# Optimization experiments

Hardware: AMD Instinct MI355X
Metric: run time of the kernel (lower is better)

The kernel has to match this reference:

```python
import jax, jax.numpy as jnp
import numpy as np

N, E = 100000, 1600000
IN, H, Z, C = 64, 128, 64, 2


def _glorot(key, fan_in, fan_out):
    s = jnp.sqrt(2.0 / (fan_in + fan_out)).astype(jnp.float32)
    return jax.random.normal(key, (fan_in, fan_out), dtype=jnp.float32) * s


def setup_inputs() -> dict:
    key = jax.random.key(0)
    ks = jax.random.split(key, 16)
    dims = [(IN, H), (H, H), (H, Z), (H, H), (H, Z), (Z, H), (H, H), (H, IN * C)]
    names = ['in', 'mu0', 'mu', 'si0', 'si', 'z', 'd0', 'out']
    inp = {
        'x': jax.random.normal(ks[0], (N, IN), dtype=jnp.float32),
        'eps': jax.random.normal(ks[1], (N, Z), dtype=jnp.float32),
        'edge_index': jax.random.randint(ks[2], (2, E), 0, N, dtype=jnp.int64),
    }
    for i, (nm, (fi, fo)) in enumerate(zip(names, dims)):
        inp[f'w_{nm}'] = _glorot(ks[3 + i], fi, fo)
        inp[f'b_{nm}'] = jnp.zeros((fo,), dtype=jnp.float32)
    return inp


def _gcn(x, W, b, src, dst, dinv):
    # PyG GCNConv: symmetric normalization with self-loops.
    h = x @ W                                      # [N, d_out]
    norm = (dinv[src] * dinv[dst])[:, None]        # [E, 1]
    agg = jax.ops.segment_sum(h[src] * norm, dst, num_segments=N)
    agg = agg + h * (dinv * dinv)[:, None]         # self-loop term (norm = 1/deg)
    return agg + b


def reference(x, edge_index, eps,
              w_in, b_in, w_mu0, b_mu0, w_mu, b_mu,
              w_si0, b_si0, w_si, b_si,
              w_z, b_z, w_d0, b_d0, w_out, b_out):
    src, dst = edge_index[0], edge_index[1]
    deg = jax.ops.segment_sum(jnp.ones((E,), jnp.float32), dst, num_segments=N) + 1.0
    dinv = jax.lax.rsqrt(deg)
    # encode
    h = jax.nn.relu(_gcn(x, w_in, b_in, src, dst, dinv))
    mu = jax.nn.relu(_gcn(h, w_mu0, b_mu0, src, dst, dinv))
    mu = jax.nn.relu(_gcn(mu, w_mu, b_mu, src, dst, dinv))
    si = jax.nn.relu(_gcn(h, w_si0, b_si0, src, dst, dinv))
    si = jax.nn.sigmoid(_gcn(si, w_si, b_si, src, dst, dinv))
    # reparameterize
    z = mu + si * eps
    # decode (first decoder layer has no activation, per the original forward)
    r = _gcn(z, w_z, b_z, src, dst, dinv)
    r = jax.nn.relu(_gcn(r, w_d0, b_d0, src, dst, dinv))
    logits = _gcn(r, w_out, b_out, src, dst, dinv)   # [N, IN*C]
    logits = logits.reshape(-1, C)                   # [N*IN, C]
    return logits, mu, si
```

## Files before the change

kernel.cpp:

```cpp
#include <hip/hip_runtime.h>


typedef short bf16x8 __attribute__((ext_vector_type(8)));
typedef float f32x4 __attribute__((ext_vector_type(4)));

__device__ __forceinline__ ushort f2bf(float f) {
    uint x = __float_as_uint(f);
    uint r = x + 0x7FFFu + ((x >> 16) & 1u);
    return (ushort)(r >> 16);
}
__device__ __forceinline__ float bf2f(ushort h) {
    return __uint_as_float(((uint)h) << 16);
}
__device__ __forceinline__ float dot2bf(uint a, uint b, float c) {
    float d;
    asm("v_dot2_f32_bf16 %0, %1, %2, %3" : "=v"(d) : "v"(a), "v"(b), "v"(c));
    return d;
}

__global__ __launch_bounds__(1024) void counts_kernel(const int* __restrict__ dst,
        int* __restrict__ deg, int* __restrict__ bc0, int E, int NB, int shift) {
    __shared__ int h[8192];
    for (int j = threadIdx.x; j < NB; j += 1024) h[j] = 0;
    __syncthreads();
    int stride = gridDim.x * 1024;
    for (int i = blockIdx.x * 1024 + threadIdx.x; i < E; i += stride) {
        int d = dst[i];
        atomicAdd(&deg[d], 1);
        atomicAdd(&h[d >> shift], 1);
    }
    __syncthreads();
    for (int j = threadIdx.x; j < NB; j += 1024) {
        int v = h[j];
        if (v) atomicAdd(&bc0[j], v);
    }
}

__global__ void dinv_kernel(const int* __restrict__ deg, float* __restrict__ dinv, int N) {
    int i = blockIdx.x * blockDim.x + threadIdx.x;
    if (i < N) dinv[i] = rsqrtf((float)(deg[i] + 1));
}

__global__ __launch_bounds__(1024) void scan_block_kernel(const int* __restrict__ in,
                                                          int* __restrict__ out,
                                                          int* __restrict__ bsum, int n) {
    __shared__ int s[1024];
    int i = blockIdx.x * 1024 + threadIdx.x;
    int v = (i < n) ? in[i] : 0;
    s[threadIdx.x] = v;
    __syncthreads();
    for (int off = 1; off < 1024; off <<= 1) {
        int t = (threadIdx.x >= off) ? s[threadIdx.x - off] : 0;
        __syncthreads();
        s[threadIdx.x] += t;
        __syncthreads();
    }
    if (i < n) out[i] = s[threadIdx.x] - v;
    if (threadIdx.x == 1023) bsum[blockIdx.x] = s[1023];
}

__global__ __launch_bounds__(1024) void scan_partials_kernel(int* __restrict__ bsum, int nb) {
    __shared__ int s[1024];
    int v = (threadIdx.x < nb) ? bsum[threadIdx.x] : 0;
    s[threadIdx.x] = v;
    __syncthreads();
    for (int off = 1; off < 1024; off <<= 1) {
        int t = (threadIdx.x >= off) ? s[threadIdx.x - off] : 0;
        __syncthreads();
        s[threadIdx.x] += t;
        __syncthreads();
    }
    if (threadIdx.x < nb) bsum[threadIdx.x] = s[threadIdx.x] - v;
}

__global__ __launch_bounds__(1024) void scan_add_kernel(int* __restrict__ arr,
                                                        const int* __restrict__ bsum, int n, int total) {
    int i = blockIdx.x * 1024 + threadIdx.x;
    if (i < n) arr[i] += bsum[blockIdx.x];
    if (i == 0) arr[n] = total;
}

__global__ void scatter_kernel(const int* __restrict__ src, const int* __restrict__ dst,
                               const int* __restrict__ bin_start, int* __restrict__ bc1,
                               int2* __restrict__ ebuf, int E, int shift) {
    int i = blockIdx.x * blockDim.x + threadIdx.x;
    if (i < E) {
        int d = dst[i];
        int b = d >> shift;
        int pos = bin_start[b] + atomicAdd(&bc1[b], 1);
        ebuf[pos] = make_int2(src[i], d);
    }
}

__global__ void place2_kernel(const int2* __restrict__ ebuf, const int* __restrict__ row_start,
                              int* __restrict__ cnt, int2* __restrict__ csr,
                              const float* __restrict__ dinv, int E) {
    int i = blockIdx.x * blockDim.x + threadIdx.x;
    if (i < E) {
        int2 e = ebuf[i];
        int pos = row_start[e.y] + atomicAdd(&cnt[e.y], 1);
        csr[pos] = make_int2(e.x, (int)(uint)f2bf(dinv[e.x] * dinv[e.y]));
    }
}

__global__ void rowsum_kernel(const int2* __restrict__ csr, const int* __restrict__ row_start,
                              const float* __restrict__ dinv, float* __restrict__ cvec, int N) {
    int j = blockIdx.x * blockDim.x + threadIdx.x;
    if (j >= N) return;
    float s = dinv[j] * dinv[j];
    int b = row_start[j], e = row_start[j + 1];
    for (int k = b; k < e; ++k) s += bf2f((ushort)((uint)csr[k].y & 0xFFFFu));
    cvec[j] = s;
}

__global__ void wcpack_kernel(const float* __restrict__ w_z, const float* __restrict__ b_z,
                              const float* __restrict__ w_d0,
                              ushort* __restrict__ P_wc, float* __restrict__ bzw) {
    int o = blockIdx.x * 256 + threadIdx.x;
    if (o >= 65 * 128) return;
    int i = o >> 7, j = o & 127;
    float s = 0.f;
    for (int k = 0; k < 128; ++k) {
        float a = (i < 64) ? w_z[i * 128 + k] : b_z[k];
        s = fmaf(a, w_d0[k * 128 + j], s);
    }
    if (i < 64) {
        int c = j >> 4, kb = i >> 5, l = ((i >> 3) & 3) * 16 + (j & 15), e = i & 7;
        P_wc[(size_t)((c * 2 + kb) * 64 + l) * 8 + e] = f2bf(s);
    } else bzw[j] = s;
}

__device__ __forceinline__ void pack_one(const float* __restrict__ W, ushort* __restrict__ P,
                                         int KI, int KO, int idx) {
    if (idx >= KI * KO) return;
    int e = idx & 7, l = (idx >> 3) & 63, t = idx >> 9;
    int KB = KI / 32;
    int c = t / KB, kb = t % KB;
    int k = kb * 32 + ((l >> 4) << 3) + e, col = c * 16 + (l & 15);
    P[idx] = f2bf(W[(size_t)k * KO + col]);
}

__global__ void megapack_kernel(const float* w_in, const float* w_mu0, const float* w_si0,
                                const float* w_mu, const float* w_si, const float* w_out,
                                ushort* P_in, ushort* P_mu0, ushort* P_si0,
                                ushort* P_mu, ushort* P_si, ushort* P_out) {
    int b = blockIdx.x, tid = threadIdx.x;
    if (b < 32)       pack_one(w_in,  P_in,  64, 128,  (b - 0)   * 256 + tid);
    else if (b < 96)  pack_one(w_mu0, P_mu0, 128, 128, (b - 32)  * 256 + tid);
    else if (b < 160) pack_one(w_si0, P_si0, 128, 128, (b - 96)  * 256 + tid);
    else if (b < 192) pack_one(w_mu,  P_mu,  128, 64,  (b - 160) * 256 + tid);
    else if (b < 224) pack_one(w_si,  P_si,  128, 64,  (b - 192) * 256 + tid);
    else              pack_one(w_out, P_out, 128, 128, (b - 224) * 256 + tid);
}

__global__ void cvt8_kernel(const float* __restrict__ in, ushort* __restrict__ out, int n8) {
    int i = blockIdx.x * 256 + threadIdx.x;
    if (i >= n8) return;
    float4 a = ((const float4*)in)[i * 2];
    float4 b = ((const float4*)in)[i * 2 + 1];
    bf16x8 o;
    o[0] = (short)f2bf(a.x); o[1] = (short)f2bf(a.y);
    o[2] = (short)f2bf(a.z); o[3] = (short)f2bf(a.w);
    o[4] = (short)f2bf(b.x); o[5] = (short)f2bf(b.y);
    o[6] = (short)f2bf(b.z); o[7] = (short)f2bf(b.w);
    ((bf16x8*)out)[i] = o;
}

template <int W, int DEPTH>
__device__ __forceinline__ void gather_pairs(float* acc, const ushort* __restrict__ xb,
        const int2* __restrict__ csr, int node, int beg, int end, int sub, int f8) {
    constexpr int SLOTS = 64 / (W / 8);
    for (int base = beg; base < end; base += 2 * SLOTS * DEPTH) {
        int sidx[DEPTH][2];
        uint wv[DEPTH][2];
        #pragma unroll
        for (int d = 0; d < DEPTH; ++d) {
            int e0 = base + 2 * (sub + SLOTS * d), e1 = e0 + 1;
            int2 p0 = csr[e0 < end ? e0 : beg];
            int2 p1 = csr[e1 < end ? e1 : beg];
            sidx[d][0] = (e0 < end) ? p0.x : node;
            sidx[d][1] = (e1 < end) ? p1.x : node;
            wv[d][0] = (e0 < end) ? (uint)p0.y : 0u;
            wv[d][1] = (e1 < end) ? (uint)p1.y : 0u;
        }
        uint4 rv[DEPTH][2];
        #pragma unroll
        for (int d = 0; d < DEPTH; ++d) {
            rv[d][0] = *(const uint4*)(xb + (size_t)sidx[d][0] * W + f8 * 8);
            rv[d][1] = *(const uint4*)(xb + (size_t)sidx[d][1] * W + f8 * 8);
        }
        #pragma unroll
        for (int d = 0; d < DEPTH; ++d) {
            uint wpk = __builtin_amdgcn_perm(wv[d][1], wv[d][0], 0x05040100u);
            uint4 v0 = rv[d][0], v1 = rv[d][1];
            uint t;
            t = __builtin_amdgcn_perm(v1.x, v0.x, 0x05040100u); acc[0] = dot2bf(t, wpk, acc[0]);
            t = __builtin_amdgcn_perm(v1.x, v0.x, 0x07060302u); acc[1] = dot2bf(t, wpk, acc[1]);
            t = __builtin_amdgcn_perm(v1.y, v0.y, 0x05040100u); acc[2] = dot2bf(t, wpk, acc[2]);
            t = __builtin_amdgcn_perm(v1.y, v0.y, 0x07060302u); acc[3] = dot2bf(t, wpk, acc[3]);
            t = __builtin_amdgcn_perm(v1.z, v0.z, 0x05040100u); acc[4] = dot2bf(t, wpk, acc[4]);
            t = __builtin_amdgcn_perm(v1.z, v0.z, 0x07060302u); acc[5] = dot2bf(t, wpk, acc[5]);
            t = __builtin_amdgcn_perm(v1.w, v0.w, 0x05040100u); acc[6] = dot2bf(t, wpk, acc[6]);
            t = __builtin_amdgcn_perm(v1.w, v0.w, 0x07060302u); acc[7] = dot2bf(t, wpk, acc[7]);
        }
    }
}

template <int W, int DEPTH>
__global__ __launch_bounds__(256) void bprop_kernel(const ushort* __restrict__ xb,
        ushort* __restrict__ out, const int* __restrict__ row_start,
        const int2* __restrict__ csr, const float* __restrict__ dinv, int N) {
    constexpr int L = W / 8;
    int wave = threadIdx.x >> 6, lane = threadIdx.x & 63;
    int node = blockIdx.x * 4 + wave;
    if (node >= N) return;
    int sub = lane / L, f8 = lane % L;
    int beg = row_start[node], end = row_start[node + 1];
    float d2 = dinv[node]; d2 *= d2;
    float acc[8] = {};
    gather_pairs<W, DEPTH>(acc, xb, csr, node, beg, end, sub, f8);
    #pragma unroll
    for (int m = L; m < 64; m <<= 1) {
        #pragma unroll
        for (int q = 0; q < 8; ++q) acc[q] += __shfl_xor(acc[q], m);
    }
    if (sub != 0) return;
    bf16x8 sv = *(const bf16x8*)(xb + (size_t)node * W + f8 * 8);
    bf16x8 oz;
    #pragma unroll
    for (int q = 0; q < 8; ++q) oz[q] = (short)f2bf(fmaf(d2, bf2f((ushort)sv[q]), acc[q]));
    *(bf16x8*)(out + (size_t)node * W + f8 * 8) = oz;
}

__global__ __launch_bounds__(256) void mssz_kernel(const ushort* __restrict__ T,
        const int* __restrict__ row_start, const int2* __restrict__ csr,
        const float* __restrict__ dinv, const float* __restrict__ b_mu,
        const float* __restrict__ b_si, const float* __restrict__ eps,
        float* __restrict__ M, float* __restrict__ S, ushort* __restrict__ zb, int N) {
    constexpr int L = 16;
    int wave = threadIdx.x >> 6, lane = threadIdx.x & 63;
    int node = blockIdx.x * 4 + wave;
    if (node >= N) return;
    int sub = lane / L, f8 = lane % L;
    int beg = row_start[node], end = row_start[node + 1];
    float d2 = dinv[node]; d2 *= d2;
    float acc[8] = {};
    gather_pairs<128, 2>(acc, T, csr, node, beg, end, sub, f8);
    #pragma unroll
    for (int m = 16; m < 64; m <<= 1) {
        #pragma unroll
        for (int q = 0; q < 8; ++q) acc[q] += __shfl_xor(acc[q], m);
    }
    if (sub != 0) return;
    bf16x8 sv = *(const bf16x8*)(T + (size_t)node * 128 + f8 * 8);
    #pragma unroll
    for (int q = 0; q < 8; ++q) acc[q] = fmaf(d2, bf2f((ushort)sv[q]), acc[q]);

    bool is_mu = (f8 < 8);
    const float* bp = is_mu ? b_mu : b_si;
    int o = (f8 & 7) * 8;
    float val[8];
    #pragma unroll
    for (int q = 0; q < 8; ++q) {
        float t = acc[q] + bp[o + q];
        val[q] = is_mu ? fmaxf(t, 0.f) : 1.f / (1.f + __expf(-t));
    }
    if (is_mu) {
        *(float4*)&M[(size_t)node * 64 + o]     = make_float4(val[0], val[1], val[2], val[3]);
        *(float4*)&M[(size_t)node * 64 + o + 4] = make_float4(val[4], val[5], val[6], val[7]);
    } else {
        *(float4*)&S[(size_t)node * 64 + o]     = make_float4(val[0], val[1], val[2], val[3]);
        *(float4*)&S[(size_t)node * 64 + o + 4] = make_float4(val[4], val[5], val[6], val[7]);
    }
    float oth[8];
    #pragma unroll
    for (int q = 0; q < 8; ++q) oth[q] = __shfl_xor(val[q], 8);
    if (is_mu) {
        float4 e0v = *(const float4*)&eps[(size_t)node * 64 + o];
        float4 e1v = *(const float4*)&eps[(size_t)node * 64 + o + 4];
        float ev[8] = {e0v.x, e0v.y, e0v.z, e0v.w, e1v.x, e1v.y, e1v.z, e1v.w};
        bf16x8 z;
        #pragma unroll
        for (int q = 0; q < 8; ++q) z[q] = (short)f2bf(fmaf(oth[q], ev[q], val[q]));
        *(bf16x8*)(zb + (size_t)node * 64 + o) = z;
    }
}

__global__ __launch_bounds__(256) void encgemm_kernel(const ushort* __restrict__ PH,
        const bf16x8* __restrict__ Pmu0, const float* __restrict__ b_mu0,
        const bf16x8* __restrict__ Pmu,
        const bf16x8* __restrict__ Psi0, const float* __restrict__ b_si0,
        const bf16x8* __restrict__ Psi,
        ushort* __restrict__ T, int N) {
    constexpr int STR = 136;
    __shared__ __align__(16) ushort Ls[64 * STR];
    int w = threadIdx.x >> 6, l = threadIdx.x & 63;
    int lr = l & 15, lk = l >> 4;
    int rowbase = blockIdx.x * 64;
    int arow = rowbase + w * 16 + lr; if (arow > N - 1) arow = N - 1;

    bf16x8 aph[4];
    const ushort* pp = PH + (size_t)arow * 128 + lk * 8;
    #pragma unroll
    for (int kb = 0; kb < 4; ++kb) aph[kb] = *(const bf16x8*)(pp + kb * 32);

    int crow0 = w * 16 + lk * 4;
    int afrow = w * 16 + lr;

    #pragma unroll
    for (int c = 0; c < 8; ++c) {
        f32x4 acc = {0.f, 0.f, 0.f, 0.f};
        #pragma unroll
        for (int kb = 0; kb < 4; ++kb)
            acc = __builtin_amdgcn_mfma_f32_16x16x32_bf16(aph[kb], Pmu0[((size_t)c * 4 + kb) * 64 + l], acc, 0, 0, 0);
        float bv = b_mu0[c * 16 + lr];
        #pragma unroll
        for (int r = 0; r < 4; ++r)
            Ls[(crow0 + r) * STR + c * 16 + lr] = f2bf(fmaxf(acc[r] + bv, 0.f));
    }
    __syncthreads();
    bf16x8 am[4];
    #pragma unroll
    for (int kb = 0; kb < 4; ++kb) am[kb] = *(const bf16x8*)&Ls[afrow * STR + kb * 32 + lk * 8];
    f32x4 tmu[4];
    #pragma unroll
    for (int c = 0; c < 4; ++c) {
        f32x4 acc = {0.f, 0.f, 0.f, 0.f};
        #pragma unroll
        for (int kb = 0; kb < 4; ++kb)
            acc = __builtin_amdgcn_mfma_f32_16x16x32_bf16(am[kb], Pmu[((size_t)c * 4 + kb) * 64 + l], acc, 0, 0, 0);
        tmu[c] = acc;
    }
    __syncthreads();
    #pragma unroll
    for (int c = 0; c < 8; ++c) {
        f32x4 acc = {0.f, 0.f, 0.f, 0.f};
        #pragma unroll
        for (int kb = 0; kb < 4; ++kb)
            acc = __builtin_amdgcn_mfma_f32_16x16x32_bf16(aph[kb], Psi0[((size_t)c * 4 + kb) * 64 + l], acc, 0, 0, 0);
        float bv = b_si0[c * 16 + lr];
        #pragma unroll
        for (int r = 0; r < 4; ++r)
            Ls[(crow0 + r) * STR + c * 16 + lr] = f2bf(fmaxf(acc[r] + bv, 0.f));
    }
    __syncthreads();
    #pragma unroll
    for (int kb = 0; kb < 4; ++kb) am[kb] = *(const bf16x8*)&Ls[afrow * STR + kb * 32 + lk * 8];
    f32x4 tsi[4];
    #pragma unroll
    for (int c = 0; c < 4; ++c) {
        f32x4 acc = {0.f, 0.f, 0.f, 0.f};
        #pragma unroll
        for (int kb = 0; kb < 4; ++kb)
            acc = __builtin_amdgcn_mfma_f32_16x16x32_bf16(am[kb], Psi[((size_t)c * 4 + kb) * 64 + l], acc, 0, 0, 0);
        tsi[c] = acc;
    }
    __syncthreads();
    #pragma unroll
    for (int c = 0; c < 4; ++c) {
        #pragma unroll
        for (int r = 0; r < 4; ++r) {
            Ls[(crow0 + r) * STR + c * 16 + lr]      = f2bf(tmu[c][r]);
            Ls[(crow0 + r) * STR + 64 + c * 16 + lr] = f2bf(tsi[c][r]);
        }
    }
    __syncthreads();
    for (int idx = threadIdx.x; idx < 64 * 16; idx += 256) {
        int row = idx >> 4, c8 = idx & 15;
        if (rowbase + row < N) {
            bf16x8 vv = *(const bf16x8*)&Ls[row * STR + c8 * 8];
            *(bf16x8*)(T + (size_t)(rowbase + row) * 128 + c8 * 8) = vv;
        }
    }
}

template <int KI, int KO, int EPI, int OUT>
__global__ __launch_bounds__(256) void mgemm_kernel(const ushort* __restrict__ Xb,
                                                    const bf16x8* __restrict__ Wp,
                                                    const float* __restrict__ bias,
                                                    const float* __restrict__ bias2,
                                                    const float* __restrict__ cvec,
                                                    void* __restrict__ outp, int ostride, int N) {
    constexpr int KB = KI / 32;
    constexpr int CT = KO / 16;
    constexpr size_t LSB = (OUT == 1) ? (size_t)64 * KO * 4 : (size_t)64 * KO * 2;
    __shared__ __align__(16) char LsRaw[LSB];

    int w = threadIdx.x >> 6, l = threadIdx.x & 63;
    int lr = l & 15, lk = l >> 4;
    int rowbase = blockIdx.x * 64;
    int r0 = rowbase + w * 16;

    int arow = r0 + lr; if (arow > N - 1) arow = N - 1;
    bf16x8 a[KB];
    const ushort* xp = Xb + (size_t)arow * KI + lk * 8;
    #pragma unroll
    for (int kb = 0; kb < KB; ++kb) a[kb] = *(const bf16x8*)(xp + kb * 32);

    float cv[4];
    if constexpr (EPI == 3) {
        #pragma unroll
        for (int r = 0; r < 4; ++r) {
            int rr = r0 + lk * 4 + r;
            cv[r] = cvec[rr < N ? rr : 0];
        }
    }

    #pragma unroll
    for (int c = 0; c < CT; ++c) {
        f32x4 acc = {0.f, 0.f, 0.f, 0.f};
        #pragma unroll
        for (int kb = 0; kb < KB; ++kb)
            acc = __builtin_amdgcn_mfma_f32_16x16x32_bf16(a[kb], Wp[((size_t)c * KB + kb) * 64 + l], acc, 0, 0, 0);
        int col = c * 16 + lr;
        float bv = 0.f, b2v = 0.f;
        if constexpr (EPI >= 1) bv = bias[col];
        if constexpr (EPI == 3) b2v = bias2[col];
        #pragma unroll
        for (int r = 0; r < 4; ++r) {
            float v = acc[r];
            if constexpr (EPI == 1) v += bv;
            if constexpr (EPI == 2) v = fmaxf(v + bv, 0.f);
            if constexpr (EPI == 3) v = fmaxf(v + cv[r] * bv + b2v, 0.f);
            int rl = w * 16 + lk * 4 + r;
            if constexpr (OUT == 0) ((ushort*)LsRaw)[(size_t)rl * KO + col] = f2bf(v);
            else                    ((float*)LsRaw)[(size_t)rl * KO + col] = v;
        }
    }
    __syncthreads();

    if constexpr (OUT == 0) {
        ushort* o = (ushort*)outp;
        constexpr int CH = 64 * KO / 8;
        for (int idx = threadIdx.x; idx < CH; idx += 256) {
            int row = idx / (KO / 8), c8 = idx % (KO / 8);
            if (rowbase + row < N)
                *(bf16x8*)(o + (size_t)(rowbase + row) * ostride + c8 * 8) = ((const bf16x8*)LsRaw)[idx];
        }
    } else {
        float* o = (float*)outp;
        constexpr int CH = 64 * KO / 4;
        for (int idx = threadIdx.x; idx < CH; idx += 256) {
            int row = idx / (KO / 4), c4 = idx % (KO / 4);
            if (rowbase + row < N)
                *(float4*)(o + (size_t)(rowbase + row) * ostride + c4 * 4) = ((const float4*)LsRaw)[idx];
        }
    }
}

extern "C" void kernel_launch(void* const* d_in, const int* in_sizes, int n_in,
                              void* d_out, int out_size, void* d_ws, size_t ws_size,
                              hipStream_t stream) {
    const float* x    = (const float*)d_in[0];
    const float* eps  = (const float*)d_in[1];
    const int*   ei   = (const int*)d_in[2];
    const float* w_in  = (const float*)d_in[3];  const float* b_in  = (const float*)d_in[4];
    const float* w_mu0 = (const float*)d_in[5];  const float* b_mu0 = (const float*)d_in[6];
    const float* w_mu  = (const float*)d_in[7];  const float* b_mu  = (const float*)d_in[8];
    const float* w_si0 = (const float*)d_in[9];  const float* b_si0 = (const float*)d_in[10];
    const float* w_si  = (const float*)d_in[11]; const float* b_si  = (const float*)d_in[12];
    const float* w_z   = (const float*)d_in[13]; const float* b_z   = (const float*)d_in[14];
    const float* w_d0  = (const float*)d_in[15]; const float* b_d0  = (const float*)d_in[16];
    const float* w_out = (const float*)d_in[17]; const float* b_out = (const float*)d_in[18];

    const int N = in_sizes[0] / 64;
    const int E = in_sizes[2] / 2;
    const int* srcI = ei;
    const int* dstI = ei + E;

    int shift = 4;
    while (((N >> shift) + 1) > 8192) shift++;
    const int NB = (N >> shift) + 1;

    auto align = [](size_t v) { return (v + 255) & ~(size_t)255; };
    char* wsp = (char*)d_ws;
    size_t off = 0;
    int*    deg       = (int*)(wsp + off);    size_t deg_off = off; off = align(off + (size_t)N * 4);
    int*    bc0       = (int*)(wsp + off);    off = align(off + (size_t)NB * 4);
    int*    bc1       = (int*)(wsp + off);    off = align(off + (size_t)NB * 4);
    size_t  zero_span = off - deg_off;
    float*  cvec      = (float*)(wsp + off);  off = align(off + (size_t)N * 4);
    int*    row_start = (int*)(wsp + off);    off = align(off + (size_t)(N + 1) * 4);
    int*    bin_start = (int*)(wsp + off);    off = align(off + (size_t)(NB + 1) * 4);
    int*    bsum      = (int*)(wsp + off);    off = align(off + 1024 * 4);
    float*  dinv      = (float*)(wsp + off);  off = align(off + (size_t)N * 4);
    float*  bzw       = (float*)(wsp + off);  off = align(off + 128 * 4);
    ushort* P_in      = (ushort*)(wsp + off); off = align(off + 64 * 128 * 2);
    ushort* P_mu0     = (ushort*)(wsp + off); off = align(off + 128 * 128 * 2);
    ushort* P_si0     = (ushort*)(wsp + off); off = align(off + 128 * 128 * 2);
    ushort* P_mu      = (ushort*)(wsp + off); off = align(off + 128 * 64 * 2);
    ushort* P_si      = (ushort*)(wsp + off); off = align(off + 128 * 64 * 2);
    ushort* P_wc      = (ushort*)(wsp + off); off = align(off + 64 * 128 * 2);
    ushort* P_out     = (ushort*)(wsp + off); off = align(off + 128 * 128 * 2);
    int2*   csr       = (int2*)(wsp + off);   off = align(off + (size_t)E * 8);
    int2*   ebuf      = (int2*)(wsp + off);   off = align(off + (size_t)E * 8);
    ushort* xb        = (ushort*)ebuf;
    ushort* B1        = (ushort*)(wsp + off); off = align(off + (size_t)N * 128 * 2);
    ushort* B1lo = B1;
    ushort* B1hi = B1 + (size_t)N * 64;

    float* Cc = (float*)d_out;
    float* M  = Cc + (size_t)N * 128;
    float* S  = M + (size_t)N * 64;
    ushort* CcLo = (ushort*)Cc;
    ushort* CcHi = (ushort*)(Cc + (size_t)N * 64);
    ushort* Db   = (ushort*)M;

    const int TB = 256;
    hipMemsetAsync(deg, 0, zero_span, stream);
    counts_kernel<<<256, 1024, 0, stream>>>(dstI, deg, bc0, E, NB, shift);
    dinv_kernel<<<(N + TB - 1) / TB, TB, 0, stream>>>(deg, dinv, N);
    int nbN = (N + 1023) / 1024;
    scan_block_kernel<<<nbN, 1024, 0, stream>>>(deg, row_start, bsum, N);
    scan_partials_kernel<<<1, 1024, 0, stream>>>(bsum, nbN);
    scan_add_kernel<<<nbN, 1024, 0, stream>>>(row_start, bsum, N, E);
    int nbB = (NB + 1023) / 1024;
    scan_block_kernel<<<nbB, 1024, 0, stream>>>(bc0, bin_start, bsum, NB);
    scan_partials_kernel<<<1, 1024, 0, stream>>>(bsum, nbB);
    scan_add_kernel<<<nbB, 1024, 0, stream>>>(bin_start, bsum, NB, E);
    hipMemsetAsync(deg, 0, (size_t)N * 4, stream);
    scatter_kernel<<<(E + TB - 1) / TB, TB, 0, stream>>>(srcI, dstI, bin_start, bc1, ebuf, E, shift);
    place2_kernel<<<(E + TB - 1) / TB, TB, 0, stream>>>(ebuf, row_start, deg, csr, dinv, E);
    rowsum_kernel<<<(N + TB - 1) / TB, TB, 0, stream>>>(csr, row_start, dinv, cvec, N);
    wcpack_kernel<<<(65 * 128 + 255) / 256, 256, 0, stream>>>(w_z, b_z, w_d0, P_wc, bzw);
    megapack_kernel<<<288, 256, 0, stream>>>(w_in, w_mu0, w_si0, w_mu, w_si, w_out,
                                             P_in, P_mu0, P_si0, P_mu, P_si, P_out);
    cvt8_kernel<<<((N * 8) + 255) / 256, 256, 0, stream>>>(x, xb, N * 8);

    int PG = (N + 3) / 4;
    int GB = (N + 63) / 64;

    bprop_kernel<64, 1><<<PG, 256, 0, stream>>>(xb, B1lo, row_start, csr, dinv, N);
    mgemm_kernel<64, 128, 2, 0><<<GB, 256, 0, stream>>>(B1lo, (const bf16x8*)P_in, b_in, nullptr, nullptr, CcLo, 128, N);
    bprop_kernel<128, 2><<<PG, 256, 0, stream>>>(CcLo, Db, row_start, csr, dinv, N);
    encgemm_kernel<<<GB, 256, 0, stream>>>(Db,
                                           (const bf16x8*)P_mu0, b_mu0, (const bf16x8*)P_mu,
                                           (const bf16x8*)P_si0, b_si0, (const bf16x8*)P_si,
                                           CcHi, N);
    mssz_kernel<<<PG, 256, 0, stream>>>(CcHi, row_start, csr, dinv, b_mu, b_si, eps, M, S, B1lo, N);
    bprop_kernel<64, 1><<<PG, 256, 0, stream>>>(B1lo, B1hi, row_start, csr, dinv, N);
    bprop_kernel<64, 1><<<PG, 256, 0, stream>>>(B1hi, xb, row_start, csr, dinv, N);
    mgemm_kernel<64, 128, 3, 0><<<GB, 256, 0, stream>>>(xb, (const bf16x8*)P_wc, bzw, b_d0, cvec, CcLo, 128, N);
    bprop_kernel<128, 2><<<PG, 256, 0, stream>>>(CcLo, B1, row_start, csr, dinv, N);
    mgemm_kernel<128, 128, 1, 1><<<GB, 256, 0, stream>>>(B1, (const bf16x8*)P_out, b_out, nullptr, nullptr, Cc, 128, N);
}
```

Baseline: 660.1 us.

## Process two nodes per wave in width-64 propagation and fold dinv into scan

Adds a pprop_kernel for the 64-wide propagation passes in which each wave handles two adjacent nodes. It issues the CSR and feature-row loads for both nodes' first chunks up front, so more independent gathers are in flight and latency is better hidden. The dinv computation also moves into the first scan_block kernel, removing one launch. The cost is higher register pressure from the duplicated staging buffers and some load imbalance when the two paired nodes have very different degrees.

Result: faster. 642.9 us (-2.6%).

```diff
diff --git a/kernel.cpp b/kernel.cpp
--- a/kernel.cpp
+++ b/kernel.cpp
@@ -36,17 +36,14 @@
     }
 }
 
-__global__ void dinv_kernel(const int* __restrict__ deg, float* __restrict__ dinv, int N) {
-    int i = blockIdx.x * blockDim.x + threadIdx.x;
-    if (i < N) dinv[i] = rsqrtf((float)(deg[i] + 1));
-}
-
 __global__ __launch_bounds__(1024) void scan_block_kernel(const int* __restrict__ in,
                                                           int* __restrict__ out,
-                                                          int* __restrict__ bsum, int n) {
+                                                          int* __restrict__ bsum,
+                                                          float* __restrict__ dinv, int n) {
     __shared__ int s[1024];
     int i = blockIdx.x * 1024 + threadIdx.x;
     int v = (i < n) ? in[i] : 0;
+    if (dinv && i < n) dinv[i] = rsqrtf((float)(v + 1));
     s[threadIdx.x] = v;
     __syncthreads();
     for (int off = 1; off < 1024; off <<= 1) {
@@ -202,6 +199,133 @@
             t = __builtin_amdgcn_perm(v1.z, v0.z, 0x07060302u); acc[5] = dot2bf(t, wpk, acc[5]);
             t = __builtin_amdgcn_perm(v1.w, v0.w, 0x05040100u); acc[6] = dot2bf(t, wpk, acc[6]);
             t = __builtin_amdgcn_perm(v1.w, v0.w, 0x07060302u); acc[7] = dot2bf(t, wpk, acc[7]);
+        }
+    }
+}
+
+template <int W>
+struct GS {
+    static constexpr int L = W / 8;
+    static constexpr int SLOTS = 64 / L;
+    static constexpr int PP = 16 / (2 * SLOTS);
+    int2 c[2 * PP];
+    uint4 r[2 * PP];
+};
+
+template <int W>
+__device__ __forceinline__ void g_csr(GS<W>& st, const int2* __restrict__ csr,
+                                      int base, int beg, int end, int sub) {
+    int safe = (end > beg) ? beg : 0;
+    #pragma unroll
+    for (int p = 0; p < GS<W>::PP; ++p) {
+        int e0 = base + 2 * (sub + GS<W>::SLOTS * p);
+        st.c[2 * p]     = csr[e0 < end ? e0 : safe];
+        st.c[2 * p + 1] = csr[e0 + 1 < end ? e0 + 1 : safe];
+    }
+}
+
+template <int W>
+__device__ __forceinline__ void g_rows(GS<W>& st, const ushort* __restrict__ xb, int f8) {
+    #pragma unroll
+    for (int i = 0; i < 2 * GS<W>::PP; ++i)
+        st.r[i] = *(const uint4*)(xb + (size_t)st.c[i].x * W + f8 * 8);
+}
+
+template <int W>
+__device__ __forceinline__ void g_consume(GS<W>& st, float* acc, int base, int end, int sub) {
+    #pragma unroll
+    for (int p = 0; p < GS<W>::PP; ++p) {
+        int e0 = base + 2 * (sub + GS<W>::SLOTS * p);
+        uint w0 = (e0 < end) ? (uint)st.c[2 * p].y : 0u;
+        uint w1 = (e0 + 1 < end) ? (uint)st.c[2 * p + 1].y : 0u;
+        uint wpk = __builtin_amdgcn_perm(w1, w0, 0x05040100u);
+        uint4 v0 = st.r[2 * p], v1 = st.r[2 * p + 1];
+        uint t;
+        t = __builtin_amdgcn_perm(v1.x, v0.x, 0x05040100u); acc[0] = dot2bf(t, wpk, acc[0]);
+        t = __builtin_amdgcn_perm(v1.x, v0.x, 0x07060302u); acc[1] = dot2bf(t, wpk, acc[1]);
+        t = __builtin_amdgcn_perm(v1.y, v0.y, 0x05040100u); acc[2] = dot2bf(t, wpk, acc[2]);
+        t = __builtin_amdgcn_perm(v1.y, v0.y, 0x07060302u); acc[3] = dot2bf(t, wpk, acc[3]);
+        t = __builtin_amdgcn_perm(v1.z, v0.z, 0x05040100u); acc[4] = dot2bf(t, wpk, acc[4]);
+        t = __builtin_amdgcn_perm(v1.z, v0.z, 0x07060302u); acc[5] = dot2bf(t, wpk, acc[5]);
+        t = __builtin_amdgcn_perm(v1.w, v0.w, 0x05040100u); acc[6] = dot2bf(t, wpk, acc[6]);
+        t = __builtin_amdgcn_perm(v1.w, v0.w, 0x07060302u); acc[7] = dot2bf(t, wpk, acc[7]);
+    }
+}
+
+template <int W>
+__global__ __launch_bounds__(256) void pprop_kernel(const ushort* __restrict__ xb,
+        ushort* __restrict__ out, const int* __restrict__ row_start,
+        const int2* __restrict__ csr, const float* __restrict__ dinv, int N) {
+    constexpr int L = W / 8;
+    int wave = threadIdx.x >> 6, lane = threadIdx.x & 63;
+    int nb = (blockIdx.x * 4 + wave) * 2;
+    if (nb >= N) return;
+    int sub = lane / L, f8 = lane % L;
+    bool v1 = (nb + 1) < N;
+    int n0 = nb, n1 = v1 ? nb + 1 : nb;
+
+    int2 rs01 = *(const int2*)&row_start[nb];
+    int rs2 = row_start[v1 ? nb + 2 : nb + 1];
+    int beg0 = rs01.x, end0 = rs01.y;
+    int beg1 = rs01.y, end1 = v1 ? rs2 : rs01.y;
+
+    float d20 = dinv[n0], d21 = dinv[n1];
+    bf16x8 sv0 = *(const bf16x8*)(xb + (size_t)n0 * W + f8 * 8);
+    bf16x8 sv1 = *(const bf16x8*)(xb + (size_t)n1 * W + f8 * 8);
+
+    GS<W> sA, sB, sA2, sB2;
+    g_csr(sA, csr, beg0, beg0, end0, sub);
+    g_csr(sB, csr, beg1, beg1, end1, sub);
+    g_csr(sA2, csr, beg0 + 16, beg0, end0, sub);
+    g_csr(sB2, csr, beg1 + 16, beg1, end1, sub);
+    g_rows(sA, xb, f8);
+    g_rows(sB, xb, f8);
+
+    float a0[8] = {}, a1[8] = {};
+    bool m0 = (beg0 + 16) < end0, m1 = (beg1 + 16) < end1;
+    g_consume(sA, a0, beg0, end0, sub);
+    if (m0) g_rows(sA2, xb, f8);
+    g_consume(sB, a1, beg1, end1, sub);
+    if (m1) g_rows(sB2, xb, f8);
+    if (m0) {
+        g_consume(sA2, a0, beg0 + 16, end0, sub);
+        for (int base = beg0 + 32; base < end0; base += 16) {
+            GS<W> t;
+            g_csr(t, csr, base, beg0, end0, sub);
+            g_rows(t, xb, f8);
+            g_consume(t, a0, base, end0, sub);
+        }
+    }
+    if (m1) {
+        g_consume(sB2, a1, beg1 + 16, end1, sub);
+        for (int base = beg1 + 32; base < end1; base += 16) {
+            GS<W> t;
+            g_csr(t, csr, base, beg1, end1, sub);
+            g_rows(t, xb, f8);
+            g_consume(t, a1, base, end1, sub);
+        }
+    }
+
+    #pragma unroll
+    for (int m = L; m < 64; m <<= 1) {
+        #pragma unroll
+        for (int q = 0; q < 8; ++q) {
+            a0[q] += __shfl_xor(a0[q], m);
+            a1[q] += __shfl_xor(a1[q], m);
+        }
+    }
+    if (sub == 0) {
+        float d2 = d20 * d20;
+        bf16x8 o0;
+        #pragma unroll
+        for (int q = 0; q < 8; ++q) o0[q] = (short)f2bf(fmaf(d2, bf2f((ushort)sv0[q]), a0[q]));
+        *(bf16x8*)(out + (size_t)n0 * W + f8 * 8) = o0;
+        if (v1) {
+            float e2 = d21 * d21;
+            bf16x8 o1;
+            #pragma unroll
+            for (int q = 0; q < 8; ++q) o1[q] = (short)f2bf(fmaf(e2, bf2f((ushort)sv1[q]), a1[q]));
+            *(bf16x8*)(out + (size_t)n1 * W + f8 * 8) = o1;
         }
     }
 }
@@ -509,13 +633,12 @@
     const int TB = 256;
     hipMemsetAsync(deg, 0, zero_span, stream);
     counts_kernel<<<256, 1024, 0, stream>>>(dstI, deg, bc0, E, NB, shift);
-    dinv_kernel<<<(N + TB - 1) / TB, TB, 0, stream>>>(deg, dinv, N);
     int nbN = (N + 1023) / 1024;
-    scan_block_kernel<<<nbN, 1024, 0, stream>>>(deg, row_start, bsum, N);
+    scan_block_kernel<<<nbN, 1024, 0, stream>>>(deg, row_start, bsum, dinv, N);
     scan_partials_kernel<<<1, 1024, 0, stream>>>(bsum, nbN);
     scan_add_kernel<<<nbN, 1024, 0, stream>>>(row_start, bsum, N, E);
     int nbB = (NB + 1023) / 1024;
-    scan_block_kernel<<<nbB, 1024, 0, stream>>>(bc0, bin_start, bsum, NB);
+    scan_block_kernel<<<nbB, 1024, 0, stream>>>(bc0, bin_start, bsum, nullptr, NB);
     scan_partials_kernel<<<1, 1024, 0, stream>>>(bsum, nbB);
     scan_add_kernel<<<nbB, 1024, 0, stream>>>(bin_start, bsum, NB, E);
     hipMemsetAsync(deg, 0, (size_t)N * 4, stream);
@@ -527,20 +650,21 @@
                                              P_in, P_mu0, P_si0, P_mu, P_si, P_out);
     cvt8_kernel<<<((N * 8) + 255) / 256, 256, 0, stream>>>(x, xb, N * 8);
 
-    int PG = (N + 3) / 4;
-    int GB = (N + 63) / 64;
-
-    bprop_kernel<64, 1><<<PG, 256, 0, stream>>>(xb, B1lo, row_start, csr, dinv, N);
+    int PGP = (N + 7) / 8;
+    int PGB = (N + 3) / 4;
+    int GB  = (N + 63) / 64;
+
+    pprop_kernel<64><<<PGP, 256, 0, stream>>>(xb, B1lo, row_start, csr, dinv, N);
     mgemm_kernel<64, 128, 2, 0><<<GB, 256, 0, stream>>>(B1lo, (const bf16x8*)P_in, b_in, nullptr, nullptr, CcLo, 128, N);
-    bprop_kernel<128, 2><<<PG, 256, 0, stream>>>(CcLo, Db, row_start, csr, dinv, N);
+    bprop_kernel<128, 2><<<PGB, 256, 0, stream>>>(CcLo, Db, row_start, csr, dinv, N);
     encgemm_kernel<<<GB, 256, 0, stream>>>(Db,
                                            (const bf16x8*)P_mu0, b_mu0, (const bf16x8*)P_mu,
                                            (const bf16x8*)P_si0, b_si0, (const bf16x8*)P_si,
                                            CcHi, N);
-    mssz_kernel<<<PG, 256, 0, stream>>>(CcHi, row_start, csr, dinv, b_mu, b_si, eps, M, S, B1lo, N);
-    bprop_kernel<64, 1><<<PG, 256, 0, stream>>>(B1lo, B1hi, row_start, csr, dinv, N);
-    bprop_kernel<64, 1><<<PG, 256, 0, stream>>>(B1hi, xb, row_start, csr, dinv, N);
+    mssz_kernel<<<PGB, 256, 0, stream>>>(CcHi, row_start, csr, dinv, b_mu, b_si, eps, M, S, B1lo, N);
+    pprop_kernel<64><<<PGP, 256, 0, stream>>>(B1lo, B1hi, row_start, csr, dinv, N);
+    pprop_kernel<64><<<PGP, 256, 0, stream>>>(B1hi, xb, row_start, csr, dinv, N);
     mgemm_kernel<64, 128, 3, 0><<<GB, 256, 0, stream>>>(xb, (const bf16x8*)P_wc, bzw, b_d0, cvec, CcLo, 128, N);
-    bprop_kernel<128, 2><<<PG, 256, 0, stream>>>(CcLo, B1, row_start, csr, dinv, N);
+    bprop_kernel<128, 2><<<PGB, 256, 0, stream>>>(CcLo, B1, row_start, csr, dinv, N);
     mgemm_kernel<128, 128, 1, 1><<<GB, 256, 0, stream>>>(B1, (const bf16x8*)P_out, b_out, nullptr, nullptr, Cc, 128, N);
 }
```
